# Optimization experiments

Hardware: AMD Instinct MI355X
Metric: run time of the kernel (lower is better)

The kernel has to match this reference:

```python
import jax, jax.numpy as jnp
import numpy as np

B = 64          # graphs per batch
NN = 4096       # nodes per graph (64x64 lattice)
N = B * NN      # total nodes
DEG = 4         # avg degree
E = N * DEG     # total directed edges
DIN, H, L = 1, 128, 64


def setup_inputs() -> dict:
    key = jax.random.key(0)
    ks = jax.random.split(key, 16)
    x = jax.random.normal(ks[0], (N, DIN), dtype=jnp.float32)
    eps = jax.random.normal(ks[1], (B, L), dtype=jnp.float32)
    # per-graph random edges, offset so they never cross graphs
    src = jax.random.randint(ks[2], (E,), 0, NN)
    dst = jax.random.randint(ks[3], (E,), 0, NN)
    off = (jnp.arange(E) // (NN * DEG)) * NN
    edge_index = jnp.stack([src + off, dst + off]).astype(jnp.int32)
    batch = (jnp.arange(N) // NN).astype(jnp.int32)
    s = 0.02
    p = lambda k, shp: s * jax.random.normal(k, shp, dtype=jnp.float32)
    return {
        "x": x, "eps": eps,
        "enc_w1": p(ks[4], (DIN, H)), "enc_b1": jnp.zeros((H,), jnp.float32),
        "enc_w2": p(ks[5], (H, H)),   "enc_b2": jnp.zeros((H,), jnp.float32),
        "mu_w": p(ks[6], (H, L)),     "mu_b": jnp.zeros((L,), jnp.float32),
        "lv_w": p(ks[7], (H, L)),     "lv_b": jnp.zeros((L,), jnp.float32),
        "zn_w": p(ks[8], (L, H)),     "zn_b": jnp.zeros((H,), jnp.float32),
        "dec_w1": p(ks[9], (H, H)),   "dec_b1": jnp.zeros((H,), jnp.float32),
        "dec_w2": p(ks[10], (H, H)),  "dec_b2": jnp.zeros((H,), jnp.float32),
        "out_w": p(ks[11], (H, 1)),   "out_b": jnp.zeros((1,), jnp.float32),
        "edge_index": edge_index, "batch": batch,
    }


def _gcn(h, w, b, row, col, norm, n):
    # PyG GCNConv: xW -> gather at row, scale by sym-norm, scatter-sum at col, + bias
    hw = h @ w
    msg = hw[row] * norm[:, None]
    return jax.ops.segment_sum(msg, col, num_segments=n) + b


def reference(x, eps, enc_w1, enc_b1, enc_w2, enc_b2, mu_w, mu_b, lv_w, lv_b,
              zn_w, zn_b, dec_w1, dec_b1, dec_w2, dec_b2, out_w, out_b,
              edge_index, batch):
    n = x.shape[0]
    b = eps.shape[0]
    nn_ = n // b
    # add self-loops, symmetric GCN normalization (shared by all convs)
    loops = jnp.arange(n, dtype=edge_index.dtype)
    row = jnp.concatenate([edge_index[0], loops])
    col = jnp.concatenate([edge_index[1], loops])
    deg = jax.ops.segment_sum(jnp.ones_like(col, dtype=x.dtype), col, num_segments=n)
    dinv = jnp.where(deg > 0, jax.lax.rsqrt(deg), 0.0)
    norm = dinv[row] * dinv[col]
    h = jax.nn.relu(_gcn(x, enc_w1, enc_b1, row, col, norm, n))
    h = jax.nn.relu(_gcn(h, enc_w2, enc_b2, row, col, norm, n))
    cnt = jax.ops.segment_sum(jnp.ones((n,), x.dtype), batch, num_segments=b)
    hg = jax.ops.segment_sum(h, batch, num_segments=b) / cnt[:, None]
    mu = hg @ mu_w + mu_b
    logvar = hg @ lv_w + lv_b
    # ---- reparameterize ----
    z = mu + jnp.exp(0.5 * logvar) * eps
    zn = z @ zn_w + zn_b          # [B, H]
    hd = zn[batch]                # [N, H]
    hd = jax.nn.relu(_gcn(hd, dec_w1, dec_b1, row, col, norm, n))
    hd = jax.nn.relu(_gcn(hd, dec_w2, dec_b2, row, col, norm, n))
    spin = jnp.tanh(hd @ out_w + out_b)   # [N, 1]
    recon = spin.reshape(b, nn_)
    return (recon, mu, logvar, z)
```

## Files before the change

### kernel.cpp

```cpp
#include <hip/hip_runtime.h>
#include <math.h>

#define NTOT 262144
#define BG   64
#define NNPG 4096
#define ET   1048576
#define EPG  16384
#define EPB  4096
#define HD   128
#define LD   64
#define NSEG 129
#define TN   256
#define MCAP ET

__device__ __forceinline__ void swz(int b, int& g, int& j){
  int xcd = b & 7, q = b >> 3;
  g = (q >> 2)*8 + xcd;
  j = q & 3;
}

__global__ void __launch_bounds__(1024) k_count(const int* __restrict__ ei,
                                                const float* __restrict__ w1,
                                                const float* __restrict__ b1,
                                                int* __restrict__ cntJ,
                                                float* __restrict__ t1, int* __restrict__ nfp,
                                                float* __restrict__ hgsum,
                                                int* __restrict__ mcnt,
                                                int* __restrict__ segU1,
                                                int* __restrict__ segU){
  __shared__ int h[NNPG];
  int tid = threadIdx.x;
  if (blockIdx.x == 256){
    for (int idx = tid; idx < BG*HD; idx += 1024) hgsum[idx] = 0.f;
    if (tid < 2) mcnt[tid] = 0;
    if (tid < 8) segU1[tid] = 0;
    if (tid < BG*8) segU[tid] = 0;
    if (tid < 128){
      float w = w1[tid], b = b1[tid];
      float t; int kind;
      if (w != 0.0f){ t = -b / w; kind = (w > 0.0f) ? 0 : 1; }
      else          { t = INFINITY; kind = 2; }
      h[tid] = kind;
      t1[tid] = t;
    }
    __syncthreads();
    if (tid == 0){
      int c = 0;
      for (int q = 0; q < 128; q++) c += (h[q] != 2) ? 1 : 0;
      nfp[0] = c;
    }
    return;
  }
  int g, j; swz(blockIdx.x, g, j);
  #pragma unroll
  for (int k = tid; k < NNPG; k += 1024) h[k] = 0;
  __syncthreads();
  int gbase = g*NNPG;
  const int4* dsts4 = (const int4*)(ei + ET + g*EPG + j*EPB);
  int4 D = dsts4[tid];
  atomicAdd(&h[D.x - gbase], 1); atomicAdd(&h[D.y - gbase], 1);
  atomicAdd(&h[D.z - gbase], 1); atomicAdd(&h[D.w - gbase], 1);
  __syncthreads();
  int* plane = cntJ + j*NTOT + gbase;
  #pragma unroll
  for (int k = tid; k < NNPG; k += 1024) plane[k] = h[k];
}

__global__ void k_dinvxd(const int* __restrict__ cntJ, const float* __restrict__ x,
                         float2* __restrict__ xd){
  int i = blockIdx.x*256 + threadIdx.x;
  int deg = cntJ[i] + cntJ[NTOT+i] + cntJ[2*NTOT+i] + cntJ[3*NTOT+i];
  xd[i] = make_float2(x[i], rsqrtf((float)deg + 1.0f));
}

__global__ void __launch_bounds__(1024) k_edge1(
    const int* __restrict__ ei, const float2* __restrict__ xd,
    float2* __restrict__ accJ)
{
  __shared__ float ax[NNPG];
  __shared__ float s1[NNPG];
  int tid = threadIdx.x;
  int g, j; swz(blockIdx.x, g, j);
  int gbase = g*NNPG;
  const int4* srcs4 = (const int4*)(ei + g*EPG + j*EPB);
  const int4* dsts4 = (const int4*)(ei + ET + g*EPG + j*EPB);
  int4 S = srcs4[tid], D = dsts4[tid];
  *(float4*)(ax + 4*tid) = make_float4(0.f,0.f,0.f,0.f);
  *(float4*)(s1 + 4*tid) = make_float4(0.f,0.f,0.f,0.f);
  __syncthreads();
  #define P1(s_, d_) { float2 sd = xd[s_]; int dl = (d_) - gbase; \
    atomicAdd(&ax[dl], sd.y * sd.x); \
    atomicAdd(&s1[dl], sd.y); }
  P1(S.x, D.x); P1(S.y, D.y); P1(S.z, D.z); P1(S.w, D.w);
  #undef P1
  __syncthreads();
  float4* ap = (float4*)(accJ + (size_t)j*NTOT + gbase);
  ap[2*tid+0] = make_float4(ax[4*tid+0], s1[4*tid+0], ax[4*tid+1], s1[4*tid+1]);
  ap[2*tid+1] = make_float4(ax[4*tid+2], s1[4*tid+2], ax[4*tid+3], s1[4*tid+3]);
}

__global__ void k_pack(const float2* __restrict__ xd, const float2* __restrict__ accJ,
                       const float* __restrict__ t1,
                       float4* __restrict__ rec, float* __restrict__ srowA,
                       int* __restrict__ segU1){
  __shared__ float ts[128];
  __shared__ int used[8];
  int tid = threadIdx.x;
  if (tid < 128) ts[tid] = t1[tid];
  if (tid < 8) used[tid] = 0;
  __syncthreads();
  int i = blockIdx.x*256 + tid;
  float2 xdv = xd[i];
  float2 a0 = accJ[0*NTOT + i], a1 = accJ[1*NTOT + i];
  float2 a2 = accJ[2*NTOT + i], a3 = accJ[3*NTOT + i];
  float axs = (a0.x + a1.x) + (a2.x + a3.x);
  float s1s = (a0.y + a1.y) + (a2.y + a3.y);
  float di = xdv.y;
  float ax = di * (di * xdv.x + axs);
  float sr = di * (di + s1s);
  int sc = 0;
  for (int q = 0; q < 128; q++) sc += (ts[q] < ax) ? 1 : 0;
  rec[i] = make_float4(di, di*ax, di*sr, __int_as_float(sc));
  srowA[i] = sr;
  atomicOr(&used[sc>>5], 1u << (sc & 31));
  __syncthreads();
  if (tid < 8 && used[tid]) atomicOr(&segU1[tid], used[tid]);
}

__global__ void __launch_bounds__(1024) k_tabrows(
    const float* __restrict__ wsrc, const float* __restrict__ bsrc,
    const float* __restrict__ w2, const int* __restrict__ segUsed,
    const int* __restrict__ nfA, float* __restrict__ ACbase)
{
  __shared__ float ws[128], bs[128], tsh[128];
  __shared__ int ks[128], rr[128];
  __shared__ float red[8][128][4];
  int g = blockIdx.x;
  int tid = threadIdx.x;
  int k = tid & 127, qg = tid >> 7;
  if (qg == 0){
    float w = wsrc[g*HD + k], b = bsrc[k];
    float t; int kind;
    if (w != 0.0f){ t = -b / w; kind = (w > 0.0f) ? 0 : 1; }
    else          { t = INFINITY; kind = 2; }
    ws[k] = w; bs[k] = b; tsh[k] = t; ks[k] = kind;
  }
  __syncthreads();
  if (qg == 0){
    float t = tsh[k];
    int r = 0;
    for (int q = 0; q < 128; q++){
      if (ks[q] != 2){
        float tq = tsh[q];
        if (tq < t || (tq == t && q < k)) r++;
      }
    }
    rr[k] = r;
  }
  float a0=0.f, c0=0.f, an=0.f, cn=0.f;
  #pragma unroll
  for (int u = 0; u < 16; u++){
    int q = qg*16 + u;
    float v = w2[q*HD + k];
    int kd = ks[q];
    float wq = ws[q], bq = bs[q];
    bool m0 = (kd == 1) || (kd == 2 && bq > 0.f);
    bool mn = (kd == 0) || (kd == 2 && bq > 0.f);
    float wv = wq*v, bv = bq*v;
    a0 += m0 ? wv : 0.f; c0 += m0 ? bv : 0.f;
    an += mn ? wv : 0.f; cn += mn ? bv : 0.f;
  }
  red[qg][k][0]=a0; red[qg][k][1]=c0; red[qg][k][2]=an; red[qg][k][3]=cn;
  __syncthreads();
  int nf = nfA[g];
  float* ACg = ACbase + (size_t)g*NSEG*256;
  int base = (k>>2)*8 + (k&3);
  if (qg == 0){
    float A0=0.f,C0=0.f,An=0.f,Cn=0.f;
    #pragma unroll
    for (int p = 0; p < 8; p++){
      A0+=red[p][k][0]; C0+=red[p][k][1]; An+=red[p][k][2]; Cn+=red[p][k][3];
    }
    ACg[base] = A0; ACg[base+4] = C0;
    ACg[(size_t)nf*256 + base] = An; ACg[(size_t)nf*256 + base + 4] = Cn;
  }
  __syncthreads();
  for (int wd = 0; wd < 5; wd++){
    unsigned m = (unsigned)segUsed[g*8 + wd];
    if (wd == 0) m &= ~1u;
    if ((nf >> 5) == wd) m &= ~(1u << (nf & 31));
    while (m){
      int bit = __ffs(m) - 1;
      m &= m - 1;
      int s = wd*32 + bit;
      float pa=0.f, pc=0.f;
      #pragma unroll
      for (int u = 0; u < 16; u++){
        int q = qg*16 + u;
        int kd = ks[q];
        bool act = (kd == 0) ? (rr[q] < s) : (kd == 1) ? (rr[q] >= s) : (bs[q] > 0.f);
        float v = act ? w2[q*HD + k] : 0.f;
        pa = fmaf(ws[q], v, pa); pc = fmaf(bs[q], v, pc);
      }
      red[qg][k][0]=pa; red[qg][k][1]=pc;
      __syncthreads();
      if (qg == 0){
        float A=0.f,C=0.f;
        #pragma unroll
        for (int p = 0; p < 8; p++){ A+=red[p][k][0]; C+=red[p][k][1]; }
        ACg[(size_t)s*256 + base] = A; ACg[(size_t)s*256 + base + 4] = C;
      }
      __syncthreads();
    }
  }
}

__global__ void __launch_bounds__(1024) k_edge2enc(
    const int* __restrict__ ei, const float4* __restrict__ rec,
    const int* __restrict__ nfp, float4* __restrict__ sums4,
    int2* __restrict__ missL, int* __restrict__ mcnt)
{
  __shared__ float sf[NNPG*4];
  __shared__ float4 sRec[NNPG];
  int g, j; swz(blockIdx.x, g, j);
  int tid = threadIdx.x;
  int gbase = g*NNPG;
  int nf = nfp[0];
  const int4* srcs4 = (const int4*)(ei + g*EPG + j*EPB);
  const int4* dsts4 = (const int4*)(ei + ET + g*EPG + j*EPB);
  int4 S = srcs4[tid], D = dsts4[tid];
  float4* sf4 = (float4*)sf;
  #pragma unroll
  for (int k = 0; k < 4; k++){
    sf4[4*tid + k] = make_float4(0.f,0.f,0.f,0.f);
    sRec[k*1024 + tid] = rec[gbase + k*1024 + tid];
  }
  __syncthreads();
  #define E1(s_, d_) { float4 r = sRec[(s_) - gbase]; int dl = (d_) - gbase; \
    int sb = __float_as_int(r.w); \
    atomicAdd(&sf[dl*4+0], r.y); atomicAdd(&sf[dl*4+1], r.x); \
    if (sb == nf) { atomicAdd(&sf[dl*4+2], r.y); atomicAdd(&sf[dl*4+3], r.x); } \
    else if (sb != 0) { int ix = atomicAdd(&mcnt[0], 1); \
      if (ix < MCAP) missL[ix] = make_int2(d_, s_); } }
  E1(S.x, D.x); E1(S.y, D.y); E1(S.z, D.z); E1(S.w, D.w);
  #undef E1
  __syncthreads();
  float4* sp = sums4 + (size_t)j*NTOT + gbase;
  #pragma unroll
  for (int k = 0; k < 4; k++) sp[4*tid + k] = sf4[4*tid + k];
}

__global__ void __launch_bounds__(256) k_enc_fin(
    const float4* __restrict__ rec, const float4* __restrict__ sums4,
    const float4* __restrict__ AC, const float* __restrict__ b2,
    const int* __restrict__ nfp, const int2* __restrict__ missL,
    const int* __restrict__ mcnt, float* __restrict__ hgsum)
{
  __shared__ float4 sS[TN];
  __shared__ float4 sRA[TN];
  __shared__ float red[256*4];
  int bid = blockIdx.x, g = bid & 63, part = bid >> 6;
  int tid = threadIdx.x, lane = tid & 31, nrow = tid >> 5;
  int base = g*NNPG + part*TN;
  int nf = nfp[0];
  {
    int i = base + tid;
    sRA[tid] = rec[i];
    float4 a = sums4[0*NTOT + i], b = sums4[1*NTOT + i];
    float4 c = sums4[2*NTOT + i], d = sums4[3*NTOT + i];
    sS[tid] = make_float4(a.x+b.x+c.x+d.x, a.y+b.y+c.y+d.y,
                          a.z+b.z+c.z+d.z, a.w+b.w+c.w+d.w);
  }
  __syncthreads();
  const float4* q0 = AC + (size_t)lane*2;
  const float4* qn = AC + ((size_t)nf*32 + lane)*2;
  float4 A0 = q0[0], C0 = q0[1], An = qn[0], Cn = qn[1];
  float4 dA = make_float4(An.x-A0.x, An.y-A0.y, An.z-A0.z, An.w-A0.w);
  float4 dC = make_float4(Cn.x-C0.x, Cn.y-C0.y, Cn.z-C0.z, Cn.w-C0.w);
  float4 bb = ((const float4*)b2)[lane];
  int mc = mcnt[0]; mc = mc < MCAP ? mc : MCAP;
  float gx=0.f, gy=0.f, gz=0.f, gw=0.f;
  for (int it = 0; it < TN/8; ++it){
    int li = it*8 + nrow;
    int i = base + li;
    float4 rA = sRA[li];
    float4 s4 = sS[li];
    float accx = fmaf(s4.x,A0.x, fmaf(s4.z,dA.x, fmaf(s4.y,C0.x, s4.w*dC.x)));
    float accy = fmaf(s4.x,A0.y, fmaf(s4.z,dA.y, fmaf(s4.y,C0.y, s4.w*dC.y)));
    float accz = fmaf(s4.x,A0.z, fmaf(s4.z,dA.z, fmaf(s4.y,C0.z, s4.w*dC.z)));
    float accw = fmaf(s4.x,A0.w, fmaf(s4.z,dA.w, fmaf(s4.y,C0.w, s4.w*dC.w)));
    if (mc > 0){
      for (int e = 0; e < mc; e++){
        int2 me = missL[e];
        if (me.x == i){
          float4 r = rec[me.y];
          int sb = __float_as_int(r.w);
          const float4* qm = AC + ((size_t)sb*32 + lane)*2;
          float4 qa = qm[0], qc = qm[1];
          accx = fmaf(r.y, qa.x-A0.x, fmaf(r.x, qc.x-C0.x, accx));
          accy = fmaf(r.y, qa.y-A0.y, fmaf(r.x, qc.y-C0.y, accy));
          accz = fmaf(r.y, qa.z-A0.z, fmaf(r.x, qc.z-C0.z, accz));
          accw = fmaf(r.y, qa.w-A0.w, fmaf(r.x, qc.w-C0.w, accw));
        }
      }
    }
    int si = __float_as_int(rA.w);
    bool m0 = (si == 0);
    float4 sa, sc;
    sa.x = m0 ? A0.x : An.x; sa.y = m0 ? A0.y : An.y; sa.z = m0 ? A0.z : An.z; sa.w = m0 ? A0.w : An.w;
    sc.x = m0 ? C0.x : Cn.x; sc.y = m0 ? C0.y : Cn.y; sc.z = m0 ? C0.z : Cn.z; sc.w = m0 ? C0.w : Cn.w;
    if (si != 0 && si != nf){
      const float4* qs = AC + ((size_t)si*32 + lane)*2;
      sa = qs[0]; sc = qs[1];
    }
    float d = rA.x, d2 = d*d, ca = rA.y*d;
    gx += fmaxf(fmaf(d, accx, fmaf(ca, sa.x, d2*sc.x)) + bb.x, 0.f);
    gy += fmaxf(fmaf(d, accy, fmaf(ca, sa.y, d2*sc.y)) + bb.y, 0.f);
    gz += fmaxf(fmaf(d, accz, fmaf(ca, sa.z, d2*sc.z)) + bb.z, 0.f);
    gw += fmaxf(fmaf(d, accw, fmaf(ca, sa.w, d2*sc.w)) + bb.w, 0.f);
  }
  __syncthreads();
  red[tid*4+0] = gx; red[tid*4+1] = gy; red[tid*4+2] = gz; red[tid*4+3] = gw;
  __syncthreads();
  if (nrow == 0){
    float tx=0.f, ty=0.f, tz=0.f, tw=0.f;
    for (int r2 = 0; r2 < 8; r2++){
      int t2 = (r2*32 + lane)*4;
      tx += red[t2]; ty += red[t2+1]; tz += red[t2+2]; tw += red[t2+3];
    }
    atomicAdd(&hgsum[g*HD + lane*4 + 0], tx);
    atomicAdd(&hgsum[g*HD + lane*4 + 1], ty);
    atomicAdd(&hgsum[g*HD + lane*4 + 2], tz);
    atomicAdd(&hgsum[g*HD + lane*4 + 3], tw);
  }
}

__global__ void __launch_bounds__(128) k_small(
    const float* __restrict__ hgsum,
    const float* __restrict__ mu_w, const float* __restrict__ mu_b,
    const float* __restrict__ lv_w, const float* __restrict__ lv_b,
    const float* __restrict__ eps,
    const float* __restrict__ zn_w, const float* __restrict__ zn_b,
    const float* __restrict__ dec_w1, const float* __restrict__ dec_b1,
    float* __restrict__ out_mu, float* __restrict__ out_lv, float* __restrict__ out_z,
    float* __restrict__ t2, float* __restrict__ ushG, int* __restrict__ nf2)
{
  int g = blockIdx.x, tid = threadIdx.x;
  __shared__ float hg[128], zsh[64], znsh[128];
  __shared__ int ks[128];
  hg[tid] = hgsum[g*HD + tid] * (1.0f/4096.0f);
  __syncthreads();
  if (tid < 64){
    int l = tid;
    float m = mu_b[l], v = lv_b[l];
    for (int k = 0; k < HD; k++){
      float hv = hg[k];
      m = fmaf(hv, mu_w[k*LD + l], m);
      v = fmaf(hv, lv_w[k*LD + l], v);
    }
    int o = g*LD + l;
    out_mu[o] = m; out_lv[o] = v;
    float zv = fmaf(expf(0.5f*v), eps[o], m);
    out_z[o] = zv; zsh[l] = zv;
  }
  __syncthreads();
  {
    int k = tid;
    float acc = zn_b[k];
    for (int l = 0; l < LD; l++) acc = fmaf(zsh[l], zn_w[l*HD + k], acc);
    znsh[k] = acc;
  }
  __syncthreads();
  float w;
  {
    int k = tid;
    float acc = 0.f;
    for (int j = 0; j < HD; j++) acc = fmaf(znsh[j], dec_w1[j*HD + k], acc);
    ushG[g*HD + k] = acc;
    w = acc;
  }
  float b = dec_b1[tid];
  float t; int kind;
  if (w != 0.0f){ t = -b / w; kind = (w > 0.0f) ? 0 : 1; }
  else          { t = INFINITY; kind = 2; }
  t2[g*HD + tid] = t; ks[tid] = kind;
  __syncthreads();
  if (tid == 0){
    int c = 0;
    for (int q = 0; q < 128; q++) c += (ks[q] != 2) ? 1 : 0;
    nf2[g] = c;
  }
}

__global__ void k_seg2(const float* __restrict__ t2, const float* __restrict__ srowA,
                       float4* __restrict__ rec, int* __restrict__ segUsed){
  __shared__ float ts[128];
  __shared__ int used[8];
  int tid = threadIdx.x;
  int i = blockIdx.x*256 + tid;
  int g = blockIdx.x >> 4;
  if (tid < 128) ts[tid] = t2[g*HD + tid];
  if (tid < 8) used[tid] = 0;
  __syncthreads();
  float a = srowA[i];
  int sc = 0;
  for (int q = 0; q < 128; q++) sc += (ts[q] < a) ? 1 : 0;
  float4 r = rec[i];
  r.y = __int_as_float(sc);
  rec[i] = r;
  atomicOr(&used[sc>>5], 1u << (sc & 31));
  __syncthreads();
  if (tid < 8 && used[tid]) atomicOr(&segUsed[g*8 + tid], used[tid]);
}

__global__ void __launch_bounds__(1024) k_edge2dec(
    const int* __restrict__ ei, const float4* __restrict__ rec,
    const int* __restrict__ nf2, float4* __restrict__ sums4,
    int2* __restrict__ missL, int* __restrict__ mcnt)
{
  __shared__ float sf[NNPG*4];
  __shared__ float4 sRec[NNPG];
  int g, j; swz(blockIdx.x, g, j);
  int tid = threadIdx.x;
  int gbase = g*NNPG;
  int nf = nf2[g];
  const int4* srcs4 = (const int4*)(ei + g*EPG + j*EPB);
  const int4* dsts4 = (const int4*)(ei + ET + g*EPG + j*EPB);
  int4 S = srcs4[tid], D = dsts4[tid];
  float4* sf4 = (float4*)sf;
  #pragma unroll
  for (int k = 0; k < 4; k++){
    sf4[4*tid + k] = make_float4(0.f,0.f,0.f,0.f);
    sRec[k*1024 + tid] = rec[gbase + k*1024 + tid];
  }
  __syncthreads();
  #define E2(s_, d_) { float4 r = sRec[(s_) - gbase]; int dl = (d_) - gbase; \
    int sb = __float_as_int(r.y); \
    atomicAdd(&sf[dl*4+0], r.z); atomicAdd(&sf[dl*4+1], r.x); \
    if (sb == nf) { atomicAdd(&sf[dl*4+2], r.z); atomicAdd(&sf[dl*4+3], r.x); } \
    else if (sb != 0) { int ix = atomicAdd(&mcnt[1], 1); \
      if (ix < MCAP) missL[ix] = make_int2(d_, s_); } }
  E2(S.x, D.x); E2(S.y, D.y); E2(S.z, D.z); E2(S.w, D.w);
  #undef E2
  __syncthreads();
  float4* sp = sums4 + (size_t)j*NTOT + gbase;
  #pragma unroll
  for (int k = 0; k < 4; k++) sp[4*tid + k] = sf4[4*tid + k];
}

__global__ void __launch_bounds__(256) k_dec_fin(
    const float4* __restrict__ rec, const float4* __restrict__ sums4,
    const float4* __restrict__ AC2, const float* __restrict__ b2,
    const float* __restrict__ ow, const float* __restrict__ ob,
    const int* __restrict__ nf2, const int2* __restrict__ missL,
    const int* __restrict__ mcnt, float* __restrict__ recon)
{
  __shared__ float4 sS[TN];
  __shared__ float4 sRA[TN];
  int bid = blockIdx.x, g = bid & 63, part = bid >> 6;
  int tid = threadIdx.x, lane = tid & 31, nrow = tid >> 5;
  int base = g*NNPG + part*TN;
  int nf = nf2[g];
  const float4* AC = AC2 + (size_t)g*NSEG*64;
  {
    int i = base + tid;
    sRA[tid] = rec[i];
    float4 a = sums4[0*NTOT + i], b = sums4[1*NTOT + i];
    float4 c = sums4[2*NTOT + i], d = sums4[3*NTOT + i];
    sS[tid] = make_float4(a.x+b.x+c.x+d.x, a.y+b.y+c.y+d.y,
                          a.z+b.z+c.z+d.z, a.w+b.w+c.w+d.w);
  }
  __syncthreads();
  const float4* q0 = AC + (size_t)lane*2;
  const float4* qn = AC + ((size_t)nf*32 + lane)*2;
  float4 A0 = q0[0], C0 = q0[1], An = qn[0], Cn = qn[1];
  float4 dA = make_float4(An.x-A0.x, An.y-A0.y, An.z-A0.z, An.w-A0.w);
  float4 dC = make_float4(Cn.x-C0.x, Cn.y-C0.y, Cn.z-C0.z, Cn.w-C0.w);
  float4 bb  = ((const float4*)b2)[lane];
  float4 owv = ((const float4*)ow)[lane];
  float obv = ob[0];
  int mc = mcnt[1]; mc = mc < MCAP ? mc : MCAP;
  for (int it = 0; it < TN/8; ++it){
    int li = it*8 + nrow;
    int i = base + li;
    float4 rA = sRA[li];
    float4 s4 = sS[li];
    float accx = fmaf(s4.x,A0.x, fmaf(s4.z,dA.x, fmaf(s4.y,C0.x, s4.w*dC.x)));
    float accy = fmaf(s4.x,A0.y, fmaf(s4.z,dA.y, fmaf(s4.y,C0.y, s4.w*dC.y)));
    float accz = fmaf(s4.x,A0.z, fmaf(s4.z,dA.z, fmaf(s4.y,C0.z, s4.w*dC.z)));
    float accw = fmaf(s4.x,A0.w, fmaf(s4.z,dA.w, fmaf(s4.y,C0.w, s4.w*dC.w)));
    if (mc > 0){
      for (int e = 0; e < mc; e++){
        int2 me = missL[e];
        if (me.x == i){
          float4 r = rec[me.y];
          int sb = __float_as_int(r.y);
          const float4* qm = AC + ((size_t)sb*32 + lane)*2;
          float4 qa = qm[0], qc = qm[1];
          accx = fmaf(r.z, qa.x-A0.x, fmaf(r.x, qc.x-C0.x, accx));
          accy = fmaf(r.z, qa.y-A0.y, fmaf(r.x, qc.y-C0.y, accy));
          accz = fmaf(r.z, qa.z-A0.z, fmaf(r.x, qc.z-C0.z, accz));
          accw = fmaf(r.z, qa.w-A0.w, fmaf(r.x, qc.w-C0.w, accw));
        }
      }
    }
    int si = __float_as_int(rA.y);
    bool m0 = (si == 0);
    float4 sa, sc;
    sa.x = m0 ? A0.x : An.x; sa.y = m0 ? A0.y : An.y; sa.z = m0 ? A0.z : An.z; sa.w = m0 ? A0.w : An.w;
    sc.x = m0 ? C0.x : Cn.x; sc.y = m0 ? C0.y : Cn.y; sc.z = m0 ? C0.z : Cn.z; sc.w = m0 ? C0.w : Cn.w;
    if (si != 0 && si != nf){
      const float4* qs = AC + ((size_t)si*32 + lane)*2;
      sa = qs[0]; sc = qs[1];
    }
    float d = rA.x, d2 = d*d, ca = rA.z*d;
    float hx = fmaxf(fmaf(d, accx, fmaf(ca, sa.x, d2*sc.x)) + bb.x, 0.f);
    float hy = fmaxf(fmaf(d, accy, fmaf(ca, sa.y, d2*sc.y)) + bb.y, 0.f);
    float hz = fmaxf(fmaf(d, accz, fmaf(ca, sa.z, d2*sc.z)) + bb.z, 0.f);
    float hw = fmaxf(fmaf(d, accw, fmaf(ca, sa.w, d2*sc.w)) + bb.w, 0.f);
    float dsum = hx*owv.x + hy*owv.y + hz*owv.z + hw*owv.w;
    for (int o2 = 16; o2 > 0; o2 >>= 1) dsum += __shfl_down(dsum, o2, 32);
    if (lane == 0) recon[i] = tanhf(dsum + obv);
  }
}

extern "C" void kernel_launch(void* const* d_in, const int* in_sizes, int n_in,
                              void* d_out, int out_size, void* d_ws, size_t ws_size,
                              hipStream_t stream){
  (void)in_sizes; (void)n_in; (void)out_size; (void)ws_size;
  const float* x      = (const float*)d_in[0];
  const float* eps    = (const float*)d_in[1];
  const float* enc_w1 = (const float*)d_in[2];
  const float* enc_b1 = (const float*)d_in[3];
  const float* enc_w2 = (const float*)d_in[4];
  const float* enc_b2 = (const float*)d_in[5];
  const float* mu_w   = (const float*)d_in[6];
  const float* mu_b   = (const float*)d_in[7];
  const float* lv_w   = (const float*)d_in[8];
  const float* lv_b   = (const float*)d_in[9];
  const float* zn_w   = (const float*)d_in[10];
  const float* zn_b   = (const float*)d_in[11];
  const float* dec_w1 = (const float*)d_in[12];
  const float* dec_b1 = (const float*)d_in[13];
  const float* dec_w2 = (const float*)d_in[14];
  const float* dec_b2 = (const float*)d_in[15];
  const float* out_w  = (const float*)d_in[16];
  const float* out_b  = (const float*)d_in[17];
  const int*   ei     = (const int*)d_in[18];

  float* out       = (float*)d_out;
  float* out_recon = out;
  float* out_mu    = out + NTOT;
  float* out_lv    = out_mu + BG*LD;
  float* out_z     = out_lv + BG*LD;

  char* w = (char*)d_ws;
  size_t off_b = 0;
  auto alloc = [&](size_t bytes)->void*{
    void* p = w + off_b;
    off_b += (bytes + 255) & ~(size_t)255;
    return p;
  };
  char*   regA   = (char*) alloc((size_t)4*NTOT*16);
  int*    cntJ   = (int*)   regA;
  float2* accJ   = (float2*)(regA + (size_t)4*NTOT*4);
  float4* sums4  = (float4*)regA;
  float2* xd     = (float2*)alloc((size_t)NTOT*8);
  float4* rec    = (float4*)alloc((size_t)NTOT*16);
  float*  srowA  = (float*) alloc((size_t)NTOT*4);
  int2*   missL  = (int2*)  alloc((size_t)MCAP*8);
  float*  t1     = (float*) alloc(128*4);
  int*    nf1    = (int*)   alloc(256);
  int*    nf2    = (int*)   alloc(BG*4);
  int*    segU1  = (int*)   alloc(8*4);
  int*    segU   = (int*)   alloc(BG*8*4);
  float*  t2     = (float*) alloc((size_t)BG*HD*4);
  float*  ushG   = (float*) alloc((size_t)BG*HD*4);
  float*  AC1    = (float*) alloc((size_t)NSEG*256*4);
  float*  AC2    = (float*) alloc((size_t)BG*NSEG*256*4);
  float*  hgsum  = (float*) alloc((size_t)BG*HD*4);
  int*    mcnt   = (int*)   alloc(256);


  k_count <<<257, 1024, 0, stream>>>(ei, enc_w1, enc_b1, cntJ, t1, nf1,
                                     hgsum, mcnt, segU1, segU);
  k_dinvxd<<<NTOT/256, 256, 0, stream>>>(cntJ, x, xd);
  k_edge1 <<<256, 1024, 0, stream>>>(ei, xd, accJ);
  k_pack  <<<NTOT/256, 256, 0, stream>>>(xd, accJ, t1, rec, srowA, segU1);
  k_tabrows<<<1, 1024, 0, stream>>>(enc_w1, enc_b1, enc_w2, segU1, nf1, AC1);

  k_edge2enc<<<256, 1024, 0, stream>>>(ei, rec, nf1, sums4, missL, mcnt);
  k_enc_fin <<<1024, 256, 0, stream>>>(rec, sums4, (const float4*)AC1, enc_b2,
                                       nf1, missL, mcnt, hgsum);

  k_small<<<BG, 128, 0, stream>>>(hgsum, mu_w, mu_b, lv_w, lv_b, eps,
                                  zn_w, zn_b, dec_w1, dec_b1,
                                  out_mu, out_lv, out_z, t2, ushG, nf2);

  k_seg2<<<NTOT/256, 256, 0, stream>>>(t2, srowA, rec, segU);

  k_tabrows<<<BG, 1024, 0, stream>>>(ushG, dec_b1, dec_w2, segU, nf2, AC2);

  k_edge2dec<<<256, 1024, 0, stream>>>(ei, rec, nf2, sums4, missL, mcnt);
  k_dec_fin <<<1024, 256, 0, stream>>>(rec, sums4, (const float4*)AC2, dec_b2,
                                       out_w, out_b, nf2, missL, mcnt, out_recon);
}
```

Baseline: 168.5 us.

## Fuse degree-norm into edge1 and run tabrows as extra blocks of edge kernels

Folds the k_dinvxd pass into k_edge1: each block computes dinv from the per-plane counts, stages the x/dinv pairs in shared memory for the source gathers, and has one j-slice write xd to global. The encoder and decoder table-row computations become extra blocks appended to k_edge2enc and k_edge2dec, with their shared memory placed in a union. This removes three kernel launches and their serialization, and lets the table build overlap with the edge scatter. The tabrows blocks are independent of the edge blocks in the same launch, so the fusion looks safe. The risk is that the 64 decoder tabrows blocks become the tail of the fused kernel.

```diff
diff --git a/kernel.cpp b/kernel.cpp
--- a/kernel.cpp
+++ b/kernel.cpp
@@ -19,124 +19,14 @@
   j = q & 3;
 }
 
-__global__ void __launch_bounds__(1024) k_count(const int* __restrict__ ei,
-                                                const float* __restrict__ w1,
-                                                const float* __restrict__ b1,
-                                                int* __restrict__ cntJ,
-                                                float* __restrict__ t1, int* __restrict__ nfp,
-                                                float* __restrict__ hgsum,
-                                                int* __restrict__ mcnt,
-                                                int* __restrict__ segU1,
-                                                int* __restrict__ segU){
-  __shared__ int h[NNPG];
-  int tid = threadIdx.x;
-  if (blockIdx.x == 256){
-    for (int idx = tid; idx < BG*HD; idx += 1024) hgsum[idx] = 0.f;
-    if (tid < 2) mcnt[tid] = 0;
-    if (tid < 8) segU1[tid] = 0;
-    if (tid < BG*8) segU[tid] = 0;
-    if (tid < 128){
-      float w = w1[tid], b = b1[tid];
-      float t; int kind;
-      if (w != 0.0f){ t = -b / w; kind = (w > 0.0f) ? 0 : 1; }
-      else          { t = INFINITY; kind = 2; }
-      h[tid] = kind;
-      t1[tid] = t;
-    }
-    __syncthreads();
-    if (tid == 0){
-      int c = 0;
-      for (int q = 0; q < 128; q++) c += (h[q] != 2) ? 1 : 0;
-      nfp[0] = c;
-    }
-    return;
-  }
-  int g, j; swz(blockIdx.x, g, j);
-  #pragma unroll
-  for (int k = tid; k < NNPG; k += 1024) h[k] = 0;
-  __syncthreads();
-  int gbase = g*NNPG;
-  const int4* dsts4 = (const int4*)(ei + ET + g*EPG + j*EPB);
-  int4 D = dsts4[tid];
-  atomicAdd(&h[D.x - gbase], 1); atomicAdd(&h[D.y - gbase], 1);
-  atomicAdd(&h[D.z - gbase], 1); atomicAdd(&h[D.w - gbase], 1);
-  __syncthreads();
-  int* plane = cntJ + j*NTOT + gbase;
-  #pragma unroll
-  for (int k = tid; k < NNPG; k += 1024) plane[k] = h[k];
-}
-
-__global__ void k_dinvxd(const int* __restrict__ cntJ, const float* __restrict__ x,
-                         float2* __restrict__ xd){
-  int i = blockIdx.x*256 + threadIdx.x;
-  int deg = cntJ[i] + cntJ[NTOT+i] + cntJ[2*NTOT+i] + cntJ[3*NTOT+i];
-  xd[i] = make_float2(x[i], rsqrtf((float)deg + 1.0f));
-}
-
-__global__ void __launch_bounds__(1024) k_edge1(
-    const int* __restrict__ ei, const float2* __restrict__ xd,
-    float2* __restrict__ accJ)
-{
-  __shared__ float ax[NNPG];
-  __shared__ float s1[NNPG];
-  int tid = threadIdx.x;
-  int g, j; swz(blockIdx.x, g, j);
-  int gbase = g*NNPG;
-  const int4* srcs4 = (const int4*)(ei + g*EPG + j*EPB);
-  const int4* dsts4 = (const int4*)(ei + ET + g*EPG + j*EPB);
-  int4 S = srcs4[tid], D = dsts4[tid];
-  *(float4*)(ax + 4*tid) = make_float4(0.f,0.f,0.f,0.f);
-  *(float4*)(s1 + 4*tid) = make_float4(0.f,0.f,0.f,0.f);
-  __syncthreads();
-  #define P1(s_, d_) { float2 sd = xd[s_]; int dl = (d_) - gbase; \
-    atomicAdd(&ax[dl], sd.y * sd.x); \
-    atomicAdd(&s1[dl], sd.y); }
-  P1(S.x, D.x); P1(S.y, D.y); P1(S.z, D.z); P1(S.w, D.w);
-  #undef P1
-  __syncthreads();
-  float4* ap = (float4*)(accJ + (size_t)j*NTOT + gbase);
-  ap[2*tid+0] = make_float4(ax[4*tid+0], s1[4*tid+0], ax[4*tid+1], s1[4*tid+1]);
-  ap[2*tid+1] = make_float4(ax[4*tid+2], s1[4*tid+2], ax[4*tid+3], s1[4*tid+3]);
-}
-
-__global__ void k_pack(const float2* __restrict__ xd, const float2* __restrict__ accJ,
-                       const float* __restrict__ t1,
-                       float4* __restrict__ rec, float* __restrict__ srowA,
-                       int* __restrict__ segU1){
-  __shared__ float ts[128];
-  __shared__ int used[8];
-  int tid = threadIdx.x;
-  if (tid < 128) ts[tid] = t1[tid];
-  if (tid < 8) used[tid] = 0;
-  __syncthreads();
-  int i = blockIdx.x*256 + tid;
-  float2 xdv = xd[i];
-  float2 a0 = accJ[0*NTOT + i], a1 = accJ[1*NTOT + i];
-  float2 a2 = accJ[2*NTOT + i], a3 = accJ[3*NTOT + i];
-  float axs = (a0.x + a1.x) + (a2.x + a3.x);
-  float s1s = (a0.y + a1.y) + (a2.y + a3.y);
-  float di = xdv.y;
-  float ax = di * (di * xdv.x + axs);
-  float sr = di * (di + s1s);
-  int sc = 0;
-  for (int q = 0; q < 128; q++) sc += (ts[q] < ax) ? 1 : 0;
-  rec[i] = make_float4(di, di*ax, di*sr, __int_as_float(sc));
-  srowA[i] = sr;
-  atomicOr(&used[sc>>5], 1u << (sc & 31));
-  __syncthreads();
-  if (tid < 8 && used[tid]) atomicOr(&segU1[tid], used[tid]);
-}
-
-__global__ void __launch_bounds__(1024) k_tabrows(
+__device__ __forceinline__ void tabrows_body(
+    int g, int tid,
     const float* __restrict__ wsrc, const float* __restrict__ bsrc,
     const float* __restrict__ w2, const int* __restrict__ segUsed,
-    const int* __restrict__ nfA, float* __restrict__ ACbase)
+    const int* __restrict__ nfA, float* __restrict__ ACbase,
+    float* ws, float* bs, float* tsh, int* ks, int* rr,
+    float (*red)[128][4])
 {
-  __shared__ float ws[128], bs[128], tsh[128];
-  __shared__ int ks[128], rr[128];
-  __shared__ float red[8][128][4];
-  int g = blockIdx.x;
-  int tid = threadIdx.x;
   int k = tid & 127, qg = tid >> 7;
   if (qg == 0){
     float w = wsrc[g*HD + k], b = bsrc[k];
@@ -215,31 +105,163 @@
   }
 }
 
+__global__ void __launch_bounds__(1024) k_count(const int* __restrict__ ei,
+                                                const float* __restrict__ w1,
+                                                const float* __restrict__ b1,
+                                                int* __restrict__ cntJ,
+                                                float* __restrict__ t1, int* __restrict__ nfp,
+                                                float* __restrict__ hgsum,
+                                                int* __restrict__ mcnt,
+                                                int* __restrict__ segU1,
+                                                int* __restrict__ segU){
+  __shared__ int h[NNPG];
+  int tid = threadIdx.x;
+  if (blockIdx.x == 256){
+    for (int idx = tid; idx < BG*HD; idx += 1024) hgsum[idx] = 0.f;
+    if (tid < 2) mcnt[tid] = 0;
+    if (tid < 8) segU1[tid] = 0;
+    if (tid < BG*8) segU[tid] = 0;
+    if (tid < 128){
+      float w = w1[tid], b = b1[tid];
+      float t; int kind;
+      if (w != 0.0f){ t = -b / w; kind = (w > 0.0f) ? 0 : 1; }
+      else          { t = INFINITY; kind = 2; }
+      h[tid] = kind;
+      t1[tid] = t;
+    }
+    __syncthreads();
+    if (tid == 0){
+      int c = 0;
+      for (int q = 0; q < 128; q++) c += (h[q] != 2) ? 1 : 0;
+      nfp[0] = c;
+    }
+    return;
+  }
+  int g, j; swz(blockIdx.x, g, j);
+  #pragma unroll
+  for (int k = tid; k < NNPG; k += 1024) h[k] = 0;
+  __syncthreads();
+  int gbase = g*NNPG;
+  const int4* dsts4 = (const int4*)(ei + ET + g*EPG + j*EPB);
+  int4 D = dsts4[tid];
+  atomicAdd(&h[D.x - gbase], 1); atomicAdd(&h[D.y - gbase], 1);
+  atomicAdd(&h[D.z - gbase], 1); atomicAdd(&h[D.w - gbase], 1);
+  __syncthreads();
+  int* plane = cntJ + j*NTOT + gbase;
+  #pragma unroll
+  for (int k = tid; k < NNPG; k += 1024) plane[k] = h[k];
+}
+
+__global__ void __launch_bounds__(1024) k_edge1(
+    const int* __restrict__ ei, const int* __restrict__ cntJ,
+    const float* __restrict__ x, float2* __restrict__ xd,
+    float2* __restrict__ accJ)
+{
+  __shared__ float2 sxd[NNPG];
+  __shared__ float ax[NNPG];
+  __shared__ float s1[NNPG];
+  int tid = threadIdx.x;
+  int g, j; swz(blockIdx.x, g, j);
+  int gbase = g*NNPG;
+  const int4* srcs4 = (const int4*)(ei + g*EPG + j*EPB);
+  const int4* dsts4 = (const int4*)(ei + ET + g*EPG + j*EPB);
+  int4 S = srcs4[tid], D = dsts4[tid];
+  {
+    int i0 = 4*tid;
+    int4 c0 = *(const int4*)(cntJ + 0*NTOT + gbase + i0);
+    int4 c1 = *(const int4*)(cntJ + 1*NTOT + gbase + i0);
+    int4 c2 = *(const int4*)(cntJ + 2*NTOT + gbase + i0);
+    int4 c3 = *(const int4*)(cntJ + 3*NTOT + gbase + i0);
+    float4 xv = *(const float4*)(x + gbase + i0);
+    float2 p0 = make_float2(xv.x, rsqrtf((float)(c0.x+c1.x+c2.x+c3.x) + 1.0f));
+    float2 p1 = make_float2(xv.y, rsqrtf((float)(c0.y+c1.y+c2.y+c3.y) + 1.0f));
+    float2 p2 = make_float2(xv.z, rsqrtf((float)(c0.z+c1.z+c2.z+c3.z) + 1.0f));
+    float2 p3 = make_float2(xv.w, rsqrtf((float)(c0.w+c1.w+c2.w+c3.w) + 1.0f));
+    sxd[i0+0] = p0; sxd[i0+1] = p1; sxd[i0+2] = p2; sxd[i0+3] = p3;
+    if (j == 0){
+      float4* xd4 = (float4*)(xd + gbase);
+      xd4[2*tid+0] = make_float4(p0.x, p0.y, p1.x, p1.y);
+      xd4[2*tid+1] = make_float4(p2.x, p2.y, p3.x, p3.y);
+    }
+    *(float4*)(ax + i0) = make_float4(0.f,0.f,0.f,0.f);
+    *(float4*)(s1 + i0) = make_float4(0.f,0.f,0.f,0.f);
+  }
+  __syncthreads();
+  #define P1(s_, d_) { float2 sd = sxd[(s_) - gbase]; int dl = (d_) - gbase; \
+    atomicAdd(&ax[dl], sd.y * sd.x); \
+    atomicAdd(&s1[dl], sd.y); }
+  P1(S.x, D.x); P1(S.y, D.y); P1(S.z, D.z); P1(S.w, D.w);
+  #undef P1
+  __syncthreads();
+  float4* ap = (float4*)(accJ + (size_t)j*NTOT + gbase);
+  ap[2*tid+0] = make_float4(ax[4*tid+0], s1[4*tid+0], ax[4*tid+1], s1[4*tid+1]);
+  ap[2*tid+1] = make_float4(ax[4*tid+2], s1[4*tid+2], ax[4*tid+3], s1[4*tid+3]);
+}
+
+__global__ void k_pack(const float2* __restrict__ xd, const float2* __restrict__ accJ,
+                       const float* __restrict__ t1,
+                       float4* __restrict__ rec, float* __restrict__ srowA,
+                       int* __restrict__ segU1){
+  __shared__ float ts[128];
+  __shared__ int used[8];
+  int tid = threadIdx.x;
+  if (tid < 128) ts[tid] = t1[tid];
+  if (tid < 8) used[tid] = 0;
+  __syncthreads();
+  int i = blockIdx.x*256 + tid;
+  float2 xdv = xd[i];
+  float2 a0 = accJ[0*NTOT + i], a1 = accJ[1*NTOT + i];
+  float2 a2 = accJ[2*NTOT + i], a3 = accJ[3*NTOT + i];
+  float axs = (a0.x + a1.x) + (a2.x + a3.x);
+  float s1s = (a0.y + a1.y) + (a2.y + a3.y);
+  float di = xdv.y;
+  float ax = di * (di * xdv.x + axs);
+  float sr = di * (di + s1s);
+  int sc = 0;
+  for (int q = 0; q < 128; q++) sc += (ts[q] < ax) ? 1 : 0;
+  rec[i] = make_float4(di, di*ax, di*sr, __int_as_float(sc));
+  srowA[i] = sr;
+  atomicOr(&used[sc>>5], 1u << (sc & 31));
+  __syncthreads();
+  if (tid < 8 && used[tid]) atomicOr(&segU1[tid], used[tid]);
+}
+
 __global__ void __launch_bounds__(1024) k_edge2enc(
     const int* __restrict__ ei, const float4* __restrict__ rec,
     const int* __restrict__ nfp, float4* __restrict__ sums4,
-    int2* __restrict__ missL, int* __restrict__ mcnt)
+    int2* __restrict__ missL, int* __restrict__ mcnt,
+    const float* __restrict__ enc_w1, const float* __restrict__ enc_b1,
+    const float* __restrict__ enc_w2, const int* __restrict__ segU1,
+    float* __restrict__ AC1)
 {
-  __shared__ float sf[NNPG*4];
-  __shared__ float4 sRec[NNPG];
+  __shared__ union {
+    struct { float sf[NNPG*4]; float4 sRec[NNPG]; } e;
+    struct { float ws[128], bs[128], tsh[128];
+             int ks[128], rr[128]; float red[8][128][4]; } t;
+  } u;
+  int tid = threadIdx.x;
+  if (blockIdx.x == 256){
+    tabrows_body(0, tid, enc_w1, enc_b1, enc_w2, segU1, nfp, AC1,
+                 u.t.ws, u.t.bs, u.t.tsh, u.t.ks, u.t.rr, u.t.red);
+    return;
+  }
   int g, j; swz(blockIdx.x, g, j);
-  int tid = threadIdx.x;
   int gbase = g*NNPG;
   int nf = nfp[0];
   const int4* srcs4 = (const int4*)(ei + g*EPG + j*EPB);
   const int4* dsts4 = (const int4*)(ei + ET + g*EPG + j*EPB);
   int4 S = srcs4[tid], D = dsts4[tid];
-  float4* sf4 = (float4*)sf;
+  float4* sf4 = (float4*)u.e.sf;
   #pragma unroll
   for (int k = 0; k < 4; k++){
     sf4[4*tid + k] = make_float4(0.f,0.f,0.f,0.f);
-    sRec[k*1024 + tid] = rec[gbase + k*1024 + tid];
-  }
-  __syncthreads();
-  #define E1(s_, d_) { float4 r = sRec[(s_) - gbase]; int dl = (d_) - gbase; \
+    u.e.sRec[k*1024 + tid] = rec[gbase + k*1024 + tid];
+  }
+  __syncthreads();
+  #define E1(s_, d_) { float4 r = u.e.sRec[(s_) - gbase]; int dl = (d_) - gbase; \
     int sb = __float_as_int(r.w); \
-    atomicAdd(&sf[dl*4+0], r.y); atomicAdd(&sf[dl*4+1], r.x); \
-    if (sb == nf) { atomicAdd(&sf[dl*4+2], r.y); atomicAdd(&sf[dl*4+3], r.x); } \
+    atomicAdd(&u.e.sf[dl*4+0], r.y); atomicAdd(&u.e.sf[dl*4+1], r.x); \
+    if (sb == nf) { atomicAdd(&u.e.sf[dl*4+2], r.y); atomicAdd(&u.e.sf[dl*4+3], r.x); } \
     else if (sb != 0) { int ix = atomicAdd(&mcnt[0], 1); \
       if (ix < MCAP) missL[ix] = make_int2(d_, s_); } }
   E1(S.x, D.x); E1(S.y, D.y); E1(S.z, D.z); E1(S.w, D.w);
@@ -416,28 +438,39 @@
 __global__ void __launch_bounds__(1024) k_edge2dec(
     const int* __restrict__ ei, const float4* __restrict__ rec,
     const int* __restrict__ nf2, float4* __restrict__ sums4,
-    int2* __restrict__ missL, int* __restrict__ mcnt)
+    int2* __restrict__ missL, int* __restrict__ mcnt,
+    const float* __restrict__ ushG, const float* __restrict__ dec_b1,
+    const float* __restrict__ dec_w2, const int* __restrict__ segU,
+    float* __restrict__ AC2)
 {
-  __shared__ float sf[NNPG*4];
-  __shared__ float4 sRec[NNPG];
+  __shared__ union {
+    struct { float sf[NNPG*4]; float4 sRec[NNPG]; } e;
+    struct { float ws[128], bs[128], tsh[128];
+             int ks[128], rr[128]; float red[8][128][4]; } t;
+  } u;
+  int tid = threadIdx.x;
+  if (blockIdx.x >= 256){
+    tabrows_body(blockIdx.x - 256, tid, ushG, dec_b1, dec_w2, segU, nf2, AC2,
+                 u.t.ws, u.t.bs, u.t.tsh, u.t.ks, u.t.rr, u.t.red);
+    return;
+  }
   int g, j; swz(blockIdx.x, g, j);
-  int tid = threadIdx.x;
   int gbase = g*NNPG;
   int nf = nf2[g];
   const int4* srcs4 = (const int4*)(ei + g*EPG + j*EPB);
   const int4* dsts4 = (const int4*)(ei + ET + g*EPG + j*EPB);
   int4 S = srcs4[tid], D = dsts4[tid];
-  float4* sf4 = (float4*)sf;
+  float4* sf4 = (float4*)u.e.sf;
   #pragma unroll
   for (int k = 0; k < 4; k++){
     sf4[4*tid + k] = make_float4(0.f,0.f,0.f,0.f);
-    sRec[k*1024 + tid] = rec[gbase + k*1024 + tid];
-  }
-  __syncthreads();
-  #define E2(s_, d_) { float4 r = sRec[(s_) - gbase]; int dl = (d_) - gbase; \
+    u.e.sRec[k*1024 + tid] = rec[gbase + k*1024 + tid];
+  }
+  __syncthreads();
+  #define E2(s_, d_) { float4 r = u.e.sRec[(s_) - gbase]; int dl = (d_) - gbase; \
     int sb = __float_as_int(r.y); \
-    atomicAdd(&sf[dl*4+0], r.z); atomicAdd(&sf[dl*4+1], r.x); \
-    if (sb == nf) { atomicAdd(&sf[dl*4+2], r.z); atomicAdd(&sf[dl*4+3], r.x); } \
+    atomicAdd(&u.e.sf[dl*4+0], r.z); atomicAdd(&u.e.sf[dl*4+1], r.x); \
+    if (sb == nf) { atomicAdd(&u.e.sf[dl*4+2], r.z); atomicAdd(&u.e.sf[dl*4+3], r.x); } \
     else if (sb != 0) { int ix = atomicAdd(&mcnt[1], 1); \
       if (ix < MCAP) missL[ix] = make_int2(d_, s_); } }
   E2(S.x, D.x); E2(S.y, D.y); E2(S.z, D.z); E2(S.w, D.w);
@@ -584,12 +617,11 @@
 
   k_count <<<257, 1024, 0, stream>>>(ei, enc_w1, enc_b1, cntJ, t1, nf1,
                                      hgsum, mcnt, segU1, segU);
-  k_dinvxd<<<NTOT/256, 256, 0, stream>>>(cntJ, x, xd);
-  k_edge1 <<<256, 1024, 0, stream>>>(ei, xd, accJ);
+  k_edge1 <<<256, 1024, 0, stream>>>(ei, cntJ, x, xd, accJ);
   k_pack  <<<NTOT/256, 256, 0, stream>>>(xd, accJ, t1, rec, srowA, segU1);
-  k_tabrows<<<1, 1024, 0, stream>>>(enc_w1, enc_b1, enc_w2, segU1, nf1, AC1);
-
-  k_edge2enc<<<256, 1024, 0, stream>>>(ei, rec, nf1, sums4, missL, mcnt);
+
+  k_edge2enc<<<257, 1024, 0, stream>>>(ei, rec, nf1, sums4, missL, mcnt,
+                                       enc_w1, enc_b1, enc_w2, segU1, AC1);
   k_enc_fin <<<1024, 256, 0, stream>>>(rec, sums4, (const float4*)AC1, enc_b2,
                                        nf1, missL, mcnt, hgsum);
 
@@ -599,9 +631,8 @@
 
   k_seg2<<<NTOT/256, 256, 0, stream>>>(t2, srowA, rec, segU);
 
-  k_tabrows<<<BG, 1024, 0, stream>>>(ushG, dec_b1, dec_w2, segU, nf2, AC2);
-
-  k_edge2dec<<<256, 1024, 0, stream>>>(ei, rec, nf2, sums4, missL, mcnt);
+  k_edge2dec<<<320, 1024, 0, stream>>>(ei, rec, nf2, sums4, missL, mcnt,
+                                       ushG, dec_b1, dec_w2, segU, AC2);
   k_dec_fin <<<1024, 256, 0, stream>>>(rec, sums4, (const float4*)AC2, dec_b2,
                                        out_w, out_b, nf2, missL, mcnt, out_recon);
 }
```

Result: slower. 181.7 us (+7.9%).
